# Performance work log

Measured on AMD Instinct MI355X. Metric: run time of the kernel, lower is better.

## Reference

```python
import math
import jax, jax.numpy as jnp
import numpy as np

B, T, D, H, KVH = 2, 2048, 2048, 16, 4
DK = D // H  # 128


def setup_inputs() -> dict:
    key = jax.random.key(0)
    ks = jax.random.split(key, 7)
    q = jax.random.normal(ks[0], (B, T, D), dtype=jnp.float32)
    k = jax.random.normal(ks[1], (B, T, D), dtype=jnp.float32)
    v = jax.random.normal(ks[2], (B, T, D), dtype=jnp.float32)
    # torch Linear weights: (out_features, in_features)
    Wq = jax.random.normal(ks[3], (D, D), dtype=jnp.float32) * 0.02
    Wk = jax.random.normal(ks[4], (KVH * DK, D), dtype=jnp.float32) * 0.02
    Wv = jax.random.normal(ks[5], (KVH * DK, D), dtype=jnp.float32) * 0.02
    Wo = jax.random.normal(ks[6], (D, D), dtype=jnp.float32) * 0.02
    # qk_norm gain, init = log(max_seq_len)
    g = jnp.full((1, H, 1, 1), math.log(2048.0), dtype=jnp.float32)
    return {"q": q, "k": k, "v": v, "Wq": Wq, "Wk": Wk, "Wv": Wv, "Wo": Wo, "g": g}


def _l2norm(x, eps=1e-12):
    # matches torch F.normalize(dim=-1): x / max(||x||, eps)
    n = jnp.sqrt(jnp.sum(x * x, axis=-1, keepdims=True))
    return x / jnp.maximum(n, eps)


def reference(q, k, v, Wq, Wk, Wv, Wo, g):
    b, tq, d = q.shape
    tk = k.shape[1]
    h = g.shape[1]
    dk = d // h
    kvh = Wk.shape[0] // dk

    Q = jnp.einsum('btd,ed->bte', q, Wq).reshape(b, tq, h, dk).transpose(0, 2, 1, 3)     # (B,H,Tq,dk)
    K = jnp.einsum('btd,ed->bte', k, Wk).reshape(b, tk, kvh, dk).transpose(0, 2, 1, 3)   # (B,KVH,Tk,dk)
    V = jnp.einsum('btd,ed->bte', v, Wv).reshape(b, tk, kvh, dk).transpose(0, 2, 1, 3)

    # QK-norm + learned per-head gain
    Q = g * _l2norm(Q)
    K = _l2norm(K)

    # GQA: repeat-interleave kv heads to match query heads (torch enable_gqa)
    rep = h // kvh
    Kr = jnp.repeat(K, rep, axis=1)
    Vr = jnp.repeat(V, rep, axis=1)

    scale = 1.0 / math.sqrt(dk)
    scores = jnp.einsum('bhqd,bhkd->bhqk', Q, Kr) * scale  # (B,H,Tq,Tk)
    causal = jnp.tril(jnp.ones((tq, tk), dtype=bool))
    scores = jnp.where(causal, scores, jnp.finfo(scores.dtype).min)
    A = jax.nn.softmax(scores, axis=-1)
    Y = jnp.einsum('bhqk,bhkd->bhqd', A, Vr)               # (B,H,Tq,dk)
    Y = Y.transpose(0, 2, 1, 3).reshape(b, tq, d)
    return jnp.einsum('btd,ed->bte', Y, Wo)
```

## Files before the change

### kernel.cpp

```cpp
#include <hip/hip_runtime.h>
#include <hip/hip_bf16.h>
#include <stdint.h>

#define B_ 2
#define T_ 2048
#define D_ 2048
#define H_ 16
#define KVH_ 4
#define DK_ 128

typedef __bf16 bf16x8 __attribute__((ext_vector_type(8)));
typedef float f32x4 __attribute__((ext_vector_type(4)));
typedef unsigned short u16x8 __attribute__((ext_vector_type(8)));

typedef __attribute__((address_space(1))) void* gas1_t;
typedef __attribute__((address_space(3))) void* gas3_t;

__device__ __forceinline__ uint16_t f2bf(float f) {
  uint32_t u = __builtin_bit_cast(uint32_t, f);
  u += 0x7FFFu + ((u >> 16) & 1u);
  return (uint16_t)(u >> 16);
}

__device__ __forceinline__ void async16(const void* g, void* l) {
  __builtin_amdgcn_global_load_lds((gas1_t)(uintptr_t)g, (gas3_t)l, 16, 0, 0);
}

__global__ __launch_bounds__(256) void k_cvt(const float* __restrict__ s,
                                             uint16_t* __restrict__ d, int n8) {
  int i = blockIdx.x * 256 + threadIdx.x;
  if (i >= n8) return;
  const float4* s4 = (const float4*)s;
  float4 a = s4[(size_t)i * 2], b = s4[(size_t)i * 2 + 1];
  union { uint16_t u[8]; uint4 v; } o;
  o.u[0] = f2bf(a.x); o.u[1] = f2bf(a.y); o.u[2] = f2bf(a.z); o.u[3] = f2bf(a.w);
  o.u[4] = f2bf(b.x); o.u[5] = f2bf(b.y); o.u[6] = f2bf(b.z); o.u[7] = f2bf(b.w);
  ((uint4*)d)[i] = o.v;
}

__global__ __launch_bounds__(256) void k_cvt_all(const float* __restrict__ q,
                                                 const float* __restrict__ k,
                                                 const float* __restrict__ v,
                                                 const float* __restrict__ wq,
                                                 const float* __restrict__ wk,
                                                 const float* __restrict__ wv,
                                                 uint16_t* __restrict__ qb,
                                                 uint16_t* __restrict__ kb,
                                                 uint16_t* __restrict__ vb,
                                                 uint16_t* __restrict__ wqb,
                                                 uint16_t* __restrict__ wkb,
                                                 uint16_t* __restrict__ wvb) {
  int gb = blockIdx.x;
  const float* s; uint16_t* d; int base;
  if (gb < 4096)        { s = q;  d = qb;  base = 0; }
  else if (gb < 8192)   { s = k;  d = kb;  base = 4096; }
  else if (gb < 12288)  { s = v;  d = vb;  base = 8192; }
  else if (gb < 14336)  { s = wq; d = wqb; base = 12288; }
  else if (gb < 14848)  { s = wk; d = wkb; base = 14336; }
  else                  { s = wv; d = wvb; base = 14848; }
  int i = (gb - base) * 256 + threadIdx.x;
  const float4* s4 = (const float4*)s;
  float4 a = s4[(size_t)i * 2], b = s4[(size_t)i * 2 + 1];
  union { uint16_t u[8]; uint4 v; } o;
  o.u[0] = f2bf(a.x); o.u[1] = f2bf(a.y); o.u[2] = f2bf(a.z); o.u[3] = f2bf(a.w);
  o.u[4] = f2bf(b.x); o.u[5] = f2bf(b.y); o.u[6] = f2bf(b.z); o.u[7] = f2bf(b.w);
  ((uint4*)d)[i] = o.v;
}

template <int WHICH>
__global__ __launch_bounds__(512, 2) void k_mm256(
    const uint16_t* __restrict__ qb, const uint16_t* __restrict__ kb,
    const uint16_t* __restrict__ vb,
    const uint16_t* __restrict__ Wqb, const uint16_t* __restrict__ Wkb,
    const uint16_t* __restrict__ Wvb,
    uint16_t* __restrict__ Qn, uint16_t* __restrict__ Kn,
    uint16_t* __restrict__ Vt, const float* __restrict__ g,
    float* __restrict__ Cout) {
  __shared__ char lds[131072];
  __shared__ float ssred[4][256];
  char* Alds = lds;
  char* Blds = lds + 65536;

  const int tid = threadIdx.x;
  const int wv = tid >> 6, lane = tid & 63;
  const int wr = wv >> 2, wc = wv & 3;
  const int lr = lane & 15, g4 = lane >> 4;

  const uint16_t *A, *W;
  int m0, n0, mode;
  if (WHICH == 1) {
    mode = 3; A = qb; W = Wqb;
    m0 = (blockIdx.x >> 3) << 8; n0 = (blockIdx.x & 7) << 8;
  } else {
    int bid = blockIdx.x;
    if (bid < 128)      { mode = 0; A = qb; W = Wqb; m0 = (bid >> 3) << 8; n0 = (bid & 7) << 8; }
    else if (bid < 160) { int lb = bid - 128; mode = 1; A = kb; W = Wkb; m0 = (lb >> 1) << 8; n0 = (lb & 1) << 8; }
    else                { int lb = bid - 160; mode = 2; A = vb; W = Wvb; m0 = (lb >> 1) << 8; n0 = (lb & 1) << 8; }
  }

  const int off0 = tid * 16;
  const int off1 = 8192 + tid * 16;
  const int row0 = off0 >> 6;
  const int j0 = ((off0 >> 4) & 3) ^ (row0 & 3);
  const uint16_t* aS0 = A + (size_t)(m0 + row0) * 2048 + j0 * 8;
  const uint16_t* aS1 = A + (size_t)(m0 + row0 + 128) * 2048 + j0 * 8;
  const uint16_t* bS0 = W + (size_t)(n0 + row0) * 2048 + j0 * 8;
  const uint16_t* bS1 = W + (size_t)(n0 + row0 + 128) * 2048 + j0 * 8;

  const int jsw = ((lane >> 4) ^ (lane & 3)) << 4;
  const int abase = (wr * 128 + lr) * 64 + jsw;
  const int bbase = (wc * 64 + lr) * 64 + jsw;

  f32x4 acc[8][4] = {};

  auto stageA = [&](int ks) {
    int sb = (ks & 3) << 14;
    async16(aS0 + ks * 32, Alds + sb + off0);
    async16(aS1 + ks * 32, Alds + sb + off1);
  };
  auto stageB = [&](int ks) {
    int sb = (ks & 3) << 14;
    async16(bS0 + ks * 32, Blds + sb + off0);
    async16(bS1 + ks * 32, Blds + sb + off1);
  };

  stageA(0); stageB(0); stageA(1); stageB(1); stageA(2); stageB(2);
  asm volatile("s_waitcnt vmcnt(8)" ::: "memory");
  __builtin_amdgcn_s_barrier();

  for (int kt = 0; kt < 64; ++kt) {
    const char* As_ = Alds + ((kt & 3) << 14);
    const char* Bs_ = Blds + ((kt & 3) << 14);
    bf16x8 a[4], b[4], a2[4];
#pragma unroll
    for (int m = 0; m < 4; ++m) a[m] = *(const bf16x8*)(As_ + abase + m * 1024);
#pragma unroll
    for (int n = 0; n < 4; ++n) b[n] = *(const bf16x8*)(Bs_ + bbase + n * 1024);
    if (kt + 3 < 64) stageA(kt + 3);
    __builtin_amdgcn_s_barrier();
    __builtin_amdgcn_s_setprio(1);
#pragma unroll
    for (int m = 0; m < 4; ++m)
#pragma unroll
      for (int n = 0; n < 4; ++n)
        acc[m][n] = __builtin_amdgcn_mfma_f32_16x16x32_bf16(a[m], b[n], acc[m][n], 0, 0, 0);
    __builtin_amdgcn_s_setprio(0);
    __builtin_amdgcn_s_barrier();
#pragma unroll
    for (int m = 0; m < 4; ++m) a2[m] = *(const bf16x8*)(As_ + abase + (m + 4) * 1024);
    if (kt + 3 < 64) stageB(kt + 3);
    __builtin_amdgcn_s_barrier();
    __builtin_amdgcn_s_setprio(1);
#pragma unroll
    for (int m = 0; m < 4; ++m)
#pragma unroll
      for (int n = 0; n < 4; ++n)
        acc[m + 4][n] = __builtin_amdgcn_mfma_f32_16x16x32_bf16(a2[m], b[n], acc[m + 4][n], 0, 0, 0);
    __builtin_amdgcn_s_setprio(0);
    if (kt < 61)       asm volatile("s_waitcnt vmcnt(8)" ::: "memory");
    else if (kt == 61) asm volatile("s_waitcnt vmcnt(4)" ::: "memory");
    else if (kt == 62) asm volatile("s_waitcnt vmcnt(0)" ::: "memory");
    __builtin_amdgcn_s_barrier();
  }

  const int bb = m0 >> 11;
  const int t0 = m0 & (T_ - 1);

  if (WHICH == 1 || mode == 3) {
#pragma unroll
    for (int m = 0; m < 8; ++m)
#pragma unroll
      for (int n = 0; n < 4; ++n)
#pragma unroll
        for (int r = 0; r < 4; ++r)
          Cout[(size_t)(m0 + wr * 128 + m * 16 + g4 * 4 + r) * 2048 +
               n0 + wc * 64 + n * 16 + lr] = acc[m][n][r];
  } else if (mode <= 1) {
    float ss[8][4];
#pragma unroll
    for (int m = 0; m < 8; ++m)
#pragma unroll
      for (int r = 0; r < 4; ++r) {
        float s = 0.f;
#pragma unroll
        for (int n = 0; n < 4; ++n) s += acc[m][n][r] * acc[m][n][r];
        ss[m][r] = s;
      }
#pragma unroll
    for (int mask = 1; mask < 16; mask <<= 1)
#pragma unroll
      for (int m = 0; m < 8; ++m)
#pragma unroll
        for (int r = 0; r < 4; ++r) ss[m][r] += __shfl_xor(ss[m][r], mask);
#pragma unroll
    for (int m = 0; m < 8; ++m)
#pragma unroll
      for (int r = 0; r < 4; ++r)
        if (lr == ((m << 2 | r) & 15))
          ssred[wc][wr * 128 + m * 16 + g4 * 4 + r] = ss[m][r];
    __syncthreads();
    uint16_t* outp = (mode == 0) ? Qn : Kn;
    const int NHv = (mode == 0) ? H_ : KVH_;
    const int h = (n0 >> 7) + (wc >> 1);
    const float gmul = (mode == 0) ? g[h] * 0.08838834764831845f : 1.0f;
    const int wp = wc & 2;
#pragma unroll
    for (int m = 0; m < 8; ++m)
#pragma unroll
      for (int r = 0; r < 4; ++r) {
        int row = wr * 128 + m * 16 + g4 * 4 + r;
        float tot = ssred[wp][row] + ssred[wp | 1][row];
        float scl = gmul / fmaxf(sqrtf(tot), 1e-12f);
        size_t base = ((size_t)(bb * NHv + h) * T_ + (t0 + row)) * 128 + (wc & 1) * 64 + lr;
#pragma unroll
        for (int n = 0; n < 4; ++n)
          outp[base + n * 16] = f2bf(acc[m][n][r] * scl);
      }
  } else {
    uint16_t (*tr)[264] = (uint16_t(*)[264])lds;
#pragma unroll
    for (int p = 0; p < 2; ++p) {
      __syncthreads();
      if ((wc >> 1) == p) {
#pragma unroll
        for (int m = 0; m < 8; ++m)
#pragma unroll
          for (int n = 0; n < 4; ++n)
#pragma unroll
            for (int r = 0; r < 4; ++r)
              tr[(wc & 1) * 64 + n * 16 + lr][wr * 128 + m * 16 + g4 * 4 + r] =
                  f2bf(acc[m][n][r]);
      }
      __syncthreads();
      int c2 = tid >> 2, rq = tid & 3;
      int h = (n0 >> 7) + p;
      uint16_t* dst = Vt + ((size_t)(bb * KVH_ + h) * 128 + c2) * T_ + t0 + rq * 64;
      const uint16_t* src = &tr[c2][rq * 64];
#pragma unroll
      for (int jj = 0; jj < 8; ++jj)
        *(u16x8*)(dst + jj * 8) = *(const u16x8*)(src + jj * 8);
    }
  }
}

__global__ __launch_bounds__(256) void k_attn(const uint16_t* __restrict__ Qn,
                                              const uint16_t* __restrict__ Kn,
                                              const uint16_t* __restrict__ Vt,
                                              uint16_t* __restrict__ Y) {
  __shared__ uint16_t Ks[64 * 128];
  __shared__ uint16_t Vs[128 * 64];
  __shared__ uint16_t Ps[4 * 16 * 32];
  const int npair = T_ / 128;
  const int pair_id = blockIdx.x % npair;
  const int bh = blockIdx.x / npair;
  const int h = bh % H_;
  const int b = bh / H_;
  const int kvh = h >> 2;
  const int qtA = pair_id;
  const int qtB = (T_ / 64) - 1 - pair_id;
  const uint16_t* Qh = Qn + ((size_t)(b * H_ + h) * T_) * 128;
  const uint16_t* Kh = Kn + ((size_t)(b * KVH_ + kvh) * T_) * 128;
  const uint16_t* Vh = Vt + ((size_t)(b * KVH_ + kvh) * 128) * T_;
  const int tid = threadIdx.x;
  const int w = tid >> 6, lane = tid & 63;
  const int lr = lane & 15;
  const int lk2 = (lane >> 4) << 4;
  const int r0 = (lane >> 4) << 2;
  const int qwA = qtA * 64 + w * 16;
  const int qwB = qtB * 64 + w * 16;
  char* Psw = (char*)Ps + w * 1024;

  bf16x8 qfA[4], qfB[4];
#pragma unroll
  for (int dblk = 0; dblk < 4; ++dblk) {
    qfA[dblk] = *(const bf16x8*)&Qh[(size_t)(qwA + lr) * 128 + dblk * 32 + (lk2 >> 1)];
    qfB[dblk] = *(const bf16x8*)&Qh[(size_t)(qwB + lr) * 128 + dblk * 32 + (lk2 >> 1)];
  }
  union { uint16_t u[8]; bf16x8 v; } ou;
#pragma unroll
  for (int j = 0; j < 8; ++j) ou.u[j] = 0x3F80;
  const bf16x8 ones = ou.v;
  f32x4 oA[8] = {}, oB[8] = {};
  f32x4 sumA = {}, sumB = {};

  auto tilecompute = [&](const bf16x8* qf, f32x4* o, f32x4* sum, int qw, int kv0) {
#pragma unroll
    for (int prr = 0; prr < 2; ++prr) {
#pragma unroll
      for (int kbi = 0; kbi < 2; ++kbi) {
        int kb = prr * 2 + kbi;
        f32x4 s = {};
#pragma unroll
        for (int dblk = 0; dblk < 4; ++dblk) {
          bf16x8 kf = *(const bf16x8*)((const char*)Ks +
              ((kb * 16 + lr) << 8) + ((dblk * 64 + lk2) ^ ((lr & 7) << 4)));
          s = __builtin_amdgcn_mfma_f32_16x16x32_bf16(qf[dblk], kf, s, 0, 0, 0);
        }
        int kval = kv0 + kb * 16 + lr;
#pragma unroll
        for (int r = 0; r < 4; ++r) {
          float pv = (kval <= qw + r0 + r) ? __expf(s[r]) : 0.0f;
          *(uint16_t*)(Psw + (r0 + r) * 64 + (((kbi * 16 + lr) * 2) ^ (r << 4))) = f2bf(pv);
        }
      }
      asm volatile("s_waitcnt lgkmcnt(0)" ::: "memory");
      bf16x8 pa = *(const bf16x8*)(Psw + lr * 64 + (lk2 ^ ((lr & 3) << 4)));
#pragma unroll
      for (int dblk = 0; dblk < 8; ++dblk) {
        bf16x8 vf = *(const bf16x8*)((const char*)Vs +
            ((dblk * 16 + lr) << 7) + ((prr * 64 + lk2) ^ ((lr & 7) << 4)));
        o[dblk] = __builtin_amdgcn_mfma_f32_16x16x32_bf16(pa, vf, o[dblk], 0, 0, 0);
      }
      *sum = __builtin_amdgcn_mfma_f32_16x16x32_bf16(pa, ones, *sum, 0, 0, 0);
    }
  };

  for (int tile = 0; tile <= qtB; ++tile) {
    const int kv0 = tile * 64;
#pragma unroll
    for (int i = 0; i < 4; ++i) {
      int off = i * 4096 + tid * 16;
      int krow = off >> 8;
      int kchunk = (off >> 4) & 15;
      int kcol = (kchunk ^ (krow & 7)) << 3;
      async16(Kh + (size_t)(kv0 + krow) * 128 + kcol, (char*)Ks + off);
      int vrow = off >> 7;
      int vchunk = (off >> 4) & 7;
      int vcol = (vchunk ^ (vrow & 7)) << 3;
      async16(Vh + (size_t)vrow * T_ + kv0 + vcol, (char*)Vs + off);
    }
    __syncthreads();
    tilecompute(qfB, oB, &sumB, qwB, kv0);
    if (tile <= qtA) tilecompute(qfA, oA, &sumA, qwA, kv0);
    __syncthreads();
  }

  auto writeout = [&](const f32x4* o, const f32x4& sum, int qw) {
#pragma unroll
    for (int r = 0; r < 4; ++r) {
      float inv = 1.0f / sum[r];
      size_t base = ((size_t)b * T_ + (qw + r0 + r)) * D_ + h * 128 + lr;
#pragma unroll
      for (int dblk = 0; dblk < 8; ++dblk)
        Y[base + dblk * 16] = f2bf(o[dblk][r] * inv);
    }
  };
  writeout(oA, sumA, qwA);
  writeout(oB, sumB, qwB);
}

extern "C" void kernel_launch(void* const* d_in, const int* in_sizes, int n_in,
                              void* d_out, int out_size, void* d_ws, size_t ws_size,
                              hipStream_t stream) {
  (void)in_sizes; (void)n_in; (void)out_size; (void)ws_size;
  const float* q  = (const float*)d_in[0];
  const float* k  = (const float*)d_in[1];
  const float* v  = (const float*)d_in[2];
  const float* Wq = (const float*)d_in[3];
  const float* Wk = (const float*)d_in[4];
  const float* Wv = (const float*)d_in[5];
  const float* Wo = (const float*)d_in[6];
  const float* g  = (const float*)d_in[7];
  float* out = (float*)d_out;
  char* ws = (char*)d_ws;
  const size_t MB = 1ull << 20;
  uint16_t* qb  = (uint16_t*)(ws);
  uint16_t* kb  = (uint16_t*)(ws + 16 * MB);
  uint16_t* vb  = (uint16_t*)(ws + 32 * MB);
  uint16_t* Wqb = (uint16_t*)(ws + 48 * MB);
  uint16_t* Wkb = (uint16_t*)(ws + 56 * MB);
  uint16_t* Wvb = (uint16_t*)(ws + 58 * MB);
  uint16_t* Kn  = (uint16_t*)(ws + 60 * MB);
  uint16_t* Vtb = (uint16_t*)(ws + 64 * MB);
  uint16_t* Qn  = (uint16_t*)d_out;
  uint16_t* Y   = qb;
  uint16_t* Wob = kb;

  k_cvt_all<<<15360, 256, 0, stream>>>(q, k, v, Wq, Wk, Wv, qb, kb, vb, Wqb, Wkb, Wvb);
  k_mm256<0><<<192, 512, 0, stream>>>(qb, kb, vb, Wqb, Wkb, Wvb, Qn, Kn, Vtb, g, nullptr);
  k_cvt<<<2048, 256, 0, stream>>>(Wo, Wob, (D_ * D_) / 8);
  k_attn<<<B_ * H_ * (T_ / 128), 256, 0, stream>>>(Qn, Kn, Vtb, Y);
  k_mm256<1><<<128, 512, 0, stream>>>(Y, nullptr, nullptr, Wob, nullptr, nullptr,
                                      nullptr, nullptr, nullptr, nullptr, out);
}
```

Before: 238.2 us.

## Restructure projection GEMM to double-buffered 64-wide K tiles

The 256x256 projection GEMM moves from a 4-stage ring of 32-wide K slices to a 2-stage double buffer of 64-wide K slices. Each iteration now runs four MFMA phases with two sub-steps over K, and the LDS layout and swizzle change to match 128-byte rows. The aim is to halve loop iterations and make each global load wider and better coalesced. The cost is a shallower prefetch: it now waits vmcnt(0) every iteration, which could expose memory latency.

```diff
diff --git a/kernel.cpp b/kernel.cpp
--- a/kernel.cpp
+++ b/kernel.cpp
@@ -78,8 +78,6 @@
     float* __restrict__ Cout) {
   __shared__ char lds[131072];
   __shared__ float ssred[4][256];
-  char* Alds = lds;
-  char* Blds = lds + 65536;
 
   const int tid = threadIdx.x;
   const int wv = tid >> 6, lane = tid & 63;
@@ -98,45 +96,45 @@
     else                { int lb = bid - 160; mode = 2; A = vb; W = Wvb; m0 = (lb >> 1) << 8; n0 = (lb & 1) << 8; }
   }
 
-  const int off0 = tid * 16;
-  const int off1 = 8192 + tid * 16;
-  const int row0 = off0 >> 6;
-  const int j0 = ((off0 >> 4) & 3) ^ (row0 & 3);
-  const uint16_t* aS0 = A + (size_t)(m0 + row0) * 2048 + j0 * 8;
-  const uint16_t* aS1 = A + (size_t)(m0 + row0 + 128) * 2048 + j0 * 8;
-  const uint16_t* bS0 = W + (size_t)(n0 + row0) * 2048 + j0 * 8;
-  const uint16_t* bS1 = W + (size_t)(n0 + row0 + 128) * 2048 + j0 * 8;
-
-  const int jsw = ((lane >> 4) ^ (lane & 3)) << 4;
-  const int abase = (wr * 128 + lr) * 64 + jsw;
-  const int bbase = (wc * 64 + lr) * 64 + jsw;
+  const int srow = tid >> 3;
+  const int scol = ((tid & 7) ^ (((tid >> 5) & 1) << 1)) * 8;
+  const uint16_t* aSrc = A + (size_t)(m0 + srow) * 2048 + scol;
+  const uint16_t* bSrc = W + (size_t)(n0 + srow) * 2048 + scol;
+  const int ldsOff = tid * 16;
+
+  auto stageA = [&](int ts) {
+    char* base = lds + ((ts & 1) << 16);
+#pragma unroll
+    for (int i = 0; i < 4; ++i)
+      async16(aSrc + ((size_t)i * 64) * 2048 + ts * 64, base + i * 8192 + ldsOff);
+  };
+  auto stageB = [&](int ts) {
+    char* base = lds + ((ts & 1) << 16) + 32768;
+#pragma unroll
+    for (int i = 0; i < 4; ++i)
+      async16(bSrc + ((size_t)i * 64) * 2048 + ts * 64, base + i * 8192 + ldsOff);
+  };
+
+  const int swl = ((lr >> 2) & 1) << 5;
+  const int colb = (g4 << 4) ^ swl;
+  const int aoff = (wr * 128 + lr) * 128 + colb;
+  const int boff = (wc * 64 + lr) * 128 + colb;
 
   f32x4 acc[8][4] = {};
 
-  auto stageA = [&](int ks) {
-    int sb = (ks & 3) << 14;
-    async16(aS0 + ks * 32, Alds + sb + off0);
-    async16(aS1 + ks * 32, Alds + sb + off1);
-  };
-  auto stageB = [&](int ks) {
-    int sb = (ks & 3) << 14;
-    async16(bS0 + ks * 32, Blds + sb + off0);
-    async16(bS1 + ks * 32, Blds + sb + off1);
-  };
-
-  stageA(0); stageB(0); stageA(1); stageB(1); stageA(2); stageB(2);
-  asm volatile("s_waitcnt vmcnt(8)" ::: "memory");
+  stageA(0); stageB(0);
+  asm volatile("s_waitcnt vmcnt(0)" ::: "memory");
   __builtin_amdgcn_s_barrier();
 
-  for (int kt = 0; kt < 64; ++kt) {
-    const char* As_ = Alds + ((kt & 3) << 14);
-    const char* Bs_ = Blds + ((kt & 3) << 14);
-    bf16x8 a[4], b[4], a2[4];
-#pragma unroll
-    for (int m = 0; m < 4; ++m) a[m] = *(const bf16x8*)(As_ + abase + m * 1024);
-#pragma unroll
-    for (int n = 0; n < 4; ++n) b[n] = *(const bf16x8*)(Bs_ + bbase + n * 1024);
-    if (kt + 3 < 64) stageA(kt + 3);
+  for (int t = 0; t < 32; ++t) {
+    const char* Ab = lds + ((t & 1) << 16);
+    const char* Bb = Ab + 32768;
+    bf16x8 a[4], b[4];
+#pragma unroll
+    for (int m = 0; m < 4; ++m) a[m] = *(const bf16x8*)(Ab + aoff + m * 2048);
+#pragma unroll
+    for (int n = 0; n < 4; ++n) b[n] = *(const bf16x8*)(Bb + boff + n * 2048);
+    if (t < 31) stageA(t + 1);
     __builtin_amdgcn_s_barrier();
     __builtin_amdgcn_s_setprio(1);
 #pragma unroll
@@ -147,19 +145,41 @@
     __builtin_amdgcn_s_setprio(0);
     __builtin_amdgcn_s_barrier();
 #pragma unroll
-    for (int m = 0; m < 4; ++m) a2[m] = *(const bf16x8*)(As_ + abase + (m + 4) * 1024);
-    if (kt + 3 < 64) stageB(kt + 3);
+    for (int m = 0; m < 4; ++m) a[m] = *(const bf16x8*)(Ab + aoff + (m + 4) * 2048);
+    if (t < 31) stageB(t + 1);
     __builtin_amdgcn_s_barrier();
     __builtin_amdgcn_s_setprio(1);
 #pragma unroll
     for (int m = 0; m < 4; ++m)
 #pragma unroll
       for (int n = 0; n < 4; ++n)
-        acc[m + 4][n] = __builtin_amdgcn_mfma_f32_16x16x32_bf16(a2[m], b[n], acc[m + 4][n], 0, 0, 0);
+        acc[m + 4][n] = __builtin_amdgcn_mfma_f32_16x16x32_bf16(a[m], b[n], acc[m + 4][n], 0, 0, 0);
     __builtin_amdgcn_s_setprio(0);
-    if (kt < 61)       asm volatile("s_waitcnt vmcnt(8)" ::: "memory");
-    else if (kt == 61) asm volatile("s_waitcnt vmcnt(4)" ::: "memory");
-    else if (kt == 62) asm volatile("s_waitcnt vmcnt(0)" ::: "memory");
+    __builtin_amdgcn_s_barrier();
+#pragma unroll
+    for (int m = 0; m < 4; ++m) a[m] = *(const bf16x8*)(Ab + aoff + m * 2048 + 64);
+#pragma unroll
+    for (int n = 0; n < 4; ++n) b[n] = *(const bf16x8*)(Bb + boff + n * 2048 + 64);
+    __builtin_amdgcn_s_barrier();
+    __builtin_amdgcn_s_setprio(1);
+#pragma unroll
+    for (int m = 0; m < 4; ++m)
+#pragma unroll
+      for (int n = 0; n < 4; ++n)
+        acc[m][n] = __builtin_amdgcn_mfma_f32_16x16x32_bf16(a[m], b[n], acc[m][n], 0, 0, 0);
+    __builtin_amdgcn_s_setprio(0);
+    __builtin_amdgcn_s_barrier();
+#pragma unroll
+    for (int m = 0; m < 4; ++m) a[m] = *(const bf16x8*)(Ab + aoff + (m + 4) * 2048 + 64);
+    __builtin_amdgcn_s_barrier();
+    __builtin_amdgcn_s_setprio(1);
+#pragma unroll
+    for (int m = 0; m < 4; ++m)
+#pragma unroll
+      for (int n = 0; n < 4; ++n)
+        acc[m + 4][n] = __builtin_amdgcn_mfma_f32_16x16x32_bf16(a[m], b[n], acc[m + 4][n], 0, 0, 0);
+    __builtin_amdgcn_s_setprio(0);
+    asm volatile("s_waitcnt vmcnt(0)" ::: "memory");
     __builtin_amdgcn_s_barrier();
   }
 
```

Result: no change. 234.2 us (-1.7%).
